# Optimization experiments

Measured on AMD Instinct MI355X. Metric: run time of the kernel, lower is better.

Reference implementation:

```python
import jax, jax.numpy as jnp
import numpy as np

S, B, C, H = 384, 2, 768, 12
CC = C // H

def setup_inputs() -> dict:
    key = jax.random.key(0)
    ks = jax.random.split(key, 8)
    x = jax.random.normal(ks[0], (S, B, C), dtype=jnp.float32)
    pe = jax.random.normal(ks[1], (S, S, B, C), dtype=jnp.float32)
    # causal mask: True where key index t > query index s (masked out)
    cm = (jnp.arange(S)[None, :] > jnp.arange(S)[:, None])[:, :, None]
    cm = jnp.broadcast_to(cm, (S, S, B))
    pm = jnp.zeros((S, S, B), dtype=bool)  # unused by the module's forward
    stdv = 1.0 / C ** 0.5
    qkv_w = jax.random.normal(ks[2], (3 * C, C), dtype=jnp.float32) * stdv
    qkv_b = jax.random.normal(ks[3], (3 * C,), dtype=jnp.float32) * stdv
    u = jax.random.uniform(ks[4], (C,), minval=-stdv, maxval=stdv, dtype=jnp.float32)
    w = jax.random.uniform(ks[5], (C,), minval=-stdv, maxval=stdv, dtype=jnp.float32)
    out_w = jax.random.normal(ks[6], (C, C), dtype=jnp.float32) * stdv
    out_b = jax.random.normal(ks[7], (C,), dtype=jnp.float32) * stdv
    return {"x": x, "pe": pe, "cm": cm, "pm": pm, "qkv_w": qkv_w,
            "qkv_b": qkv_b, "u": u, "w": w, "out_w": out_w, "out_b": out_b}

def reference(x, pe, cm, pm, qkv_w, qkv_b, u, w, out_w, out_b):
    s, b, c = x.shape
    qkv = x @ qkv_w.T + qkv_b                       # (s,b,3c)
    q, k, v = jnp.split(qkv, 3, axis=-1)
    q = q.reshape(s, b, H, CC)
    k = k.reshape(s, b, H, CC)
    v = v.reshape(s, b, H, CC)
    uh = u.reshape(1, 1, H, CC)
    wh = w.reshape(1, 1, H, CC)
    # content-content scores with global content bias u
    dd_ud = jnp.einsum('sbhc,tbhc->stbh', q + uh, k)
    # content-position scores against dense pairwise pe
    pe5 = pe.reshape(s, s, b, H, CC)
    dp_wp = jnp.einsum('sbhc,stbhc->stbh', q + wh, pe5)
    scale = 1.0 / CC ** 0.5
    a = (dd_ud + dp_wp) * scale
    a = jnp.where(cm[..., None], -jnp.inf, a)       # causal mask (intended)
    p = jax.nn.softmax(a, axis=1)                   # softmax over key axis t
    o = jnp.einsum('stbh,tbhc->sbhc', p, v).reshape(s, b, c)
    return o @ out_w.T + out_b
```

## Files before the change

kernel.cpp:

```cpp
#include <hip/hip_runtime.h>
#include <hip/hip_bf16.h>
#include <cstdint>

constexpr int kS  = 384;
constexpr int kB  = 2;
constexpr int kC  = 768;
constexpr int kH  = 12;
constexpr int kCC = 64;
constexpr int kHPB = 4;

typedef __attribute__((ext_vector_type(8))) short short8;
typedef __attribute__((ext_vector_type(4))) float f32x4;
typedef __attribute__((ext_vector_type(4))) unsigned short u16x4;
typedef const __attribute__((address_space(1))) unsigned int glb_u32_t;
typedef __attribute__((address_space(3))) unsigned int lds_u32_t;

static __device__ __forceinline__ ushort f2bf(float f) {
  __hip_bfloat16 h = __float2bfloat16(f);
  return *reinterpret_cast<ushort*>(&h);
}

__global__ __launch_bounds__(256) void convert_bf16(
    const float* __restrict__ x, const float* __restrict__ qw,
    const float* __restrict__ ow, ushort* __restrict__ xb,
    ushort* __restrict__ qwb, ushort* __restrict__ owb) {
  int idx = blockIdx.x * 256 + threadIdx.x;
  const float* src;
  ushort* dst;
  if (idx < 147456) {
    src = x; dst = xb;
  } else if (idx < 147456 + 442368) {
    idx -= 147456; src = qw; dst = qwb;
  } else {
    idx -= 589824; src = ow; dst = owb;
  }
  f32x4 v = *reinterpret_cast<const f32x4*>(src + (size_t)idx * 4);
  u16x4 o;
  o[0] = f2bf(v[0]); o[1] = f2bf(v[1]); o[2] = f2bf(v[2]); o[3] = f2bf(v[3]);
  *reinterpret_cast<u16x4*>(dst + (size_t)idx * 4) = o;
}

__global__ __launch_bounds__(256) void gemm_bf16_lds(
    const ushort* __restrict__ Abf, const ushort* __restrict__ Wbf,
    const float* __restrict__ bias, float* __restrict__ Cg,
    int M, int N, int K) {
  __shared__ ushort As[64 * 64];
  __shared__ ushort Ws[64 * 64];
  const int tid = threadIdx.x;
  const int m0 = blockIdx.y * 64, n0 = blockIdx.x * 64;
  const int wv = tid >> 6, l = tid & 63;
  const int wr = wv >> 1, wc = wv & 1;
  const int lr = l & 15, lk = l >> 4;

  f32x4 acc[2][2] = {{{0.f, 0.f, 0.f, 0.f}, {0.f, 0.f, 0.f, 0.f}},
                     {{0.f, 0.f, 0.f, 0.f}, {0.f, 0.f, 0.f, 0.f}}};

  for (int k0 = 0; k0 < K; k0 += 64) {
    __syncthreads();
#pragma unroll
    for (int j = 0; j < 2; ++j) {
      int cid = (j * 4 + wv) * 64 + l;
      int r = cid >> 3, c = cid & 7;
      int cs = c ^ (r & 7);
      const ushort* ga = Abf + (size_t)(m0 + r) * K + k0 + cs * 8;
      __builtin_amdgcn_global_load_lds((glb_u32_t*)ga,
                                       (lds_u32_t*)&As[(cid & ~63) * 8],
                                       16, 0, 0);
      const ushort* gw = Wbf + (size_t)(n0 + r) * K + k0 + cs * 8;
      __builtin_amdgcn_global_load_lds((glb_u32_t*)gw,
                                       (lds_u32_t*)&Ws[(cid & ~63) * 8],
                                       16, 0, 0);
    }
    __syncthreads();
#pragma unroll
    for (int ks = 0; ks < 2; ++ks) {
      short8 af[2], bw[2];
#pragma unroll
      for (int f = 0; f < 2; ++f) {
        int ra = wr * 32 + f * 16 + lr;
        int ca = (ks * 4 + lk) ^ (ra & 7);
        af[f] = *reinterpret_cast<const short8*>(&As[(ra * 8 + ca) * 8]);
        int rb = wc * 32 + f * 16 + lr;
        int cb = (ks * 4 + lk) ^ (rb & 7);
        bw[f] = *reinterpret_cast<const short8*>(&Ws[(rb * 8 + cb) * 8]);
      }
#pragma unroll
      for (int fr = 0; fr < 2; ++fr)
#pragma unroll
        for (int fc = 0; fc < 2; ++fc)
          acc[fr][fc] = __builtin_amdgcn_mfma_f32_16x16x32_bf16(
              af[fr], bw[fc], acc[fr][fc], 0, 0, 0);
    }
  }

#pragma unroll
  for (int fr = 0; fr < 2; ++fr)
#pragma unroll
    for (int fc = 0; fc < 2; ++fc)
#pragma unroll
      for (int j = 0; j < 4; ++j) {
        int m = m0 + wr * 32 + fr * 16 + lk * 4 + j;
        int n = n0 + wc * 32 + fc * 16 + lr;
        Cg[(size_t)m * N + n] = acc[fr][fc][j] + bias[n];
      }
}

__global__ __launch_bounds__(256, 6) void attn_kernel(
    const float* __restrict__ qkv, const float* __restrict__ pe,
    const float* __restrict__ u, const float* __restrict__ w,
    ushort* __restrict__ obf) {
  __shared__ float sc[kHPB][kS];

  const int bid = blockIdx.x;
  const int sb = bid / (kH / kHPB);
  const int hg = bid % (kH / kHPB);
  const int s = kS - 1 - (sb >> 1);
  const int b = sb & 1;
  const int wave = threadIdx.x >> 6;
  const int h = hg * kHPB + wave;
  const int lane = threadIdx.x & 63;
  const int tq = lane >> 4;
  const int cq = (lane & 15) * 4;
  const int ch = h * kCC + cq;
  const float scale = 0.125f;

  const int row = s * kB + b;
  const float4 q4 = *(const float4*)&qkv[(int64_t)row * 3 * kC + ch];
  const float4 u4 = *(const float4*)&u[ch];
  const float4 w4 = *(const float4*)&w[ch];
  float4 qu, qw;
  qu.x = q4.x + u4.x; qu.y = q4.y + u4.y; qu.z = q4.z + u4.z; qu.w = q4.w + u4.w;
  qw.x = q4.x + w4.x; qw.y = q4.y + w4.y; qw.z = q4.z + w4.z; qw.w = q4.w + w4.w;

  const float* kbase = qkv + (int64_t)b * 3 * kC + kC + ch;
  const float* vbase = qkv + (int64_t)b * 3 * kC + 2 * kC + ch;
  const float* pbase = pe + ((int64_t)s * kS * kB + b) * kC + ch;
  const int kstride = kB * 3 * kC;
  const int pstride = kB * kC;

  const int nfull = (s + 1) & ~15;

  int t0 = 0;
  for (; t0 < nfull; t0 += 16) {
    float4 k4[4];
    f32x4 p4[4];
#pragma unroll
    for (int i = 0; i < 4; ++i) {
      int t = t0 + i * 4 + tq;
      k4[i] = *(const float4*)&kbase[(int64_t)t * kstride];
      p4[i] = __builtin_nontemporal_load(
          (const f32x4*)&pbase[(int64_t)t * pstride]);
    }
#pragma unroll
    for (int i = 0; i < 4; ++i) {
      float r = qu.x * k4[i].x + qu.y * k4[i].y + qu.z * k4[i].z +
                qu.w * k4[i].w + qw.x * p4[i][0] + qw.y * p4[i][1] +
                qw.z * p4[i][2] + qw.w * p4[i][3];
      r += __shfl_xor(r, 1);
      r += __shfl_xor(r, 2);
      r += __shfl_xor(r, 4);
      r += __shfl_xor(r, 8);
      if ((lane & 15) == 0) sc[wave][t0 + i * 4 + tq] = r * scale;
    }
  }
  for (; t0 <= s; t0 += 4) {
    int t = t0 + tq;
    int tc = (t <= s) ? t : s;
    float4 k4 = *(const float4*)&kbase[(int64_t)tc * kstride];
    float4 p4 = *(const float4*)&pbase[(int64_t)tc * pstride];
    float r = qu.x * k4.x + qu.y * k4.y + qu.z * k4.z + qu.w * k4.w +
              qw.x * p4.x + qw.y * p4.y + qw.z * p4.z + qw.w * p4.w;
    r += __shfl_xor(r, 1);
    r += __shfl_xor(r, 2);
    r += __shfl_xor(r, 4);
    r += __shfl_xor(r, 8);
    if ((lane & 15) == 0 && t <= s) sc[wave][t] = r * scale;
  }
  __syncthreads();

  float mx = -1e30f;
  for (int t = lane; t <= s; t += 64) mx = fmaxf(mx, sc[wave][t]);
#pragma unroll
  for (int off = 32; off; off >>= 1) mx = fmaxf(mx, __shfl_xor(mx, off, 64));
  float sum = 0.f;
  for (int t = lane; t <= s; t += 64) {
    float e = __expf(sc[wave][t] - mx);
    sc[wave][t] = e;
    sum += e;
  }
#pragma unroll
  for (int off = 32; off; off >>= 1) sum += __shfl_xor(sum, off, 64);
  const float rden = 1.0f / sum;

  float4 oa = {0.f, 0.f, 0.f, 0.f};
  t0 = 0;
  for (; t0 < nfull; t0 += 16) {
    float4 v4[4];
    float p[4];
#pragma unroll
    for (int i = 0; i < 4; ++i) {
      int t = t0 + i * 4 + tq;
      v4[i] = *(const float4*)&vbase[(int64_t)t * kstride];
      p[i] = sc[wave][t];
    }
#pragma unroll
    for (int i = 0; i < 4; ++i) {
      oa.x += p[i] * v4[i].x; oa.y += p[i] * v4[i].y;
      oa.z += p[i] * v4[i].z; oa.w += p[i] * v4[i].w;
    }
  }
  for (; t0 <= s; t0 += 4) {
    int t = t0 + tq;
    if (t <= s) {
      float p = sc[wave][t];
      float4 v4 = *(const float4*)&vbase[(int64_t)t * kstride];
      oa.x += p * v4.x; oa.y += p * v4.y; oa.z += p * v4.z; oa.w += p * v4.w;
    }
  }
#pragma unroll
  for (int off = 16; off <= 32; off <<= 1) {
    oa.x += __shfl_xor(oa.x, off);
    oa.y += __shfl_xor(oa.y, off);
    oa.z += __shfl_xor(oa.z, off);
    oa.w += __shfl_xor(oa.w, off);
  }
  if (lane < 16) {
    u16x4 res;
    res[0] = f2bf(oa.x * rden); res[1] = f2bf(oa.y * rden);
    res[2] = f2bf(oa.z * rden); res[3] = f2bf(oa.w * rden);
    *reinterpret_cast<u16x4*>(&obf[(int64_t)row * kC + ch]) = res;
  }
}

extern "C" void kernel_launch(void* const* d_in, const int* in_sizes, int n_in,
                              void* d_out, int out_size, void* d_ws,
                              size_t ws_size, hipStream_t stream) {
  const float* x     = (const float*)d_in[0];
  const float* pe    = (const float*)d_in[1];
  const float* qkv_w = (const float*)d_in[4];
  const float* qkv_b = (const float*)d_in[5];
  const float* u     = (const float*)d_in[6];
  const float* w     = (const float*)d_in[7];
  const float* out_w = (const float*)d_in[8];
  const float* out_b = (const float*)d_in[9];
  float* out = (float*)d_out;

  char* wsb = (char*)d_ws;
  float*  qkv  = (float*)wsb;
  ushort* xb   = (ushort*)(wsb + 7077888);
  ushort* qwb  = (ushort*)(wsb + 8257536);
  ushort* owb  = (ushort*)(wsb + 11796480);
  ushort* obf  = (ushort*)(wsb + 12976128);

  convert_bf16<<<2880, 256, 0, stream>>>(x, qkv_w, out_w, xb, qwb, owb);

  gemm_bf16_lds<<<dim3(3 * kC / 64, kS * kB / 64), 256, 0, stream>>>(
      xb, qwb, qkv_b, qkv, kS * kB, 3 * kC, kC);

  attn_kernel<<<kS * kB * (kH / kHPB), kHPB * 64, 0, stream>>>(
      qkv, pe, u, w, obf);

  gemm_bf16_lds<<<dim3(kC / 64, kS * kB / 64), 256, 0, stream>>>(
      obf, owb, out_b, out, kS * kB, kC, kC);
}
```

Before: 137.2 us.

## Fuse attention into single-pass online softmax with DPP row reductions

Replaces the three-pass attention (scores into LDS, softmax, then PV) with a single streaming loop. The loop reads K, PE and V together and keeps an online softmax per lane group, with a lazy rescale threshold. The 16-lane score reductions move from __shfl_xor to DPP row operations, and the LDS buffer and block barrier are removed. In exchange, the loop is unrolled 2 instead of 4 per iteration, which means fewer loads in flight. Each step also pays for more exp calls and branches.

```diff
diff --git a/kernel.cpp b/kernel.cpp
--- a/kernel.cpp
+++ b/kernel.cpp
@@ -18,6 +18,20 @@
 static __device__ __forceinline__ ushort f2bf(float f) {
   __hip_bfloat16 h = __float2bfloat16(f);
   return *reinterpret_cast<ushort*>(&h);
+}
+
+template <int CTRL>
+static __device__ __forceinline__ float dpp_add(float x) {
+  int xi = __builtin_bit_cast(int, x);
+  int yi = __builtin_amdgcn_update_dpp(0, xi, CTRL, 0xF, 0xF, true);
+  return x + __builtin_bit_cast(float, yi);
+}
+static __device__ __forceinline__ float row16_sum(float x) {
+  x = dpp_add<0xB1>(x);
+  x = dpp_add<0x4E>(x);
+  x = dpp_add<0x124>(x);
+  x = dpp_add<0x128>(x);
+  return x;
 }
 
 __global__ __launch_bounds__(256) void convert_bf16(
@@ -109,8 +123,6 @@
     const float* __restrict__ qkv, const float* __restrict__ pe,
     const float* __restrict__ u, const float* __restrict__ w,
     ushort* __restrict__ obf) {
-  __shared__ float sc[kHPB][kS];
-
   const int bid = blockIdx.x;
   const int sb = bid / (kH / kHPB);
   const int hg = bid % (kH / kHPB);
@@ -125,12 +137,11 @@
   const float scale = 0.125f;
 
   const int row = s * kB + b;
-  const float4 q4 = *(const float4*)&qkv[(int64_t)row * 3 * kC + ch];
-  const float4 u4 = *(const float4*)&u[ch];
-  const float4 w4 = *(const float4*)&w[ch];
-  float4 qu, qw;
-  qu.x = q4.x + u4.x; qu.y = q4.y + u4.y; qu.z = q4.z + u4.z; qu.w = q4.w + u4.w;
-  qw.x = q4.x + w4.x; qw.y = q4.y + w4.y; qw.z = q4.z + w4.z; qw.w = q4.w + w4.w;
+  const f32x4 q4 = *(const f32x4*)&qkv[(int64_t)row * 3 * kC + ch];
+  const f32x4 u4 = *(const f32x4*)&u[ch];
+  const f32x4 w4 = *(const f32x4*)&w[ch];
+  const f32x4 qu = q4 + u4;
+  const f32x4 qw = q4 + w4;
 
   const float* kbase = qkv + (int64_t)b * 3 * kC + kC + ch;
   const float* vbase = qkv + (int64_t)b * 3 * kC + 2 * kC + ch;
@@ -138,96 +149,61 @@
   const int kstride = kB * 3 * kC;
   const int pstride = kB * kC;
 
-  const int nfull = (s + 1) & ~15;
-
-  int t0 = 0;
-  for (; t0 < nfull; t0 += 16) {
-    float4 k4[4];
-    f32x4 p4[4];
-#pragma unroll
-    for (int i = 0; i < 4; ++i) {
+  float m = -1e30f, l = 0.f;
+  f32x4 oa = {0.f, 0.f, 0.f, 0.f};
+
+  for (int t0 = 0; t0 <= s; t0 += 8) {
+    f32x4 k4[2], p4[2], v4[2];
+    int tt[2];
+#pragma unroll
+    for (int i = 0; i < 2; ++i) {
       int t = t0 + i * 4 + tq;
-      k4[i] = *(const float4*)&kbase[(int64_t)t * kstride];
+      tt[i] = t;
+      int tc = (t <= s) ? t : s;
+      k4[i] = *(const f32x4*)&kbase[(int64_t)tc * kstride];
       p4[i] = __builtin_nontemporal_load(
-          (const f32x4*)&pbase[(int64_t)t * pstride]);
-    }
-#pragma unroll
-    for (int i = 0; i < 4; ++i) {
-      float r = qu.x * k4[i].x + qu.y * k4[i].y + qu.z * k4[i].z +
-                qu.w * k4[i].w + qw.x * p4[i][0] + qw.y * p4[i][1] +
-                qw.z * p4[i][2] + qw.w * p4[i][3];
-      r += __shfl_xor(r, 1);
-      r += __shfl_xor(r, 2);
-      r += __shfl_xor(r, 4);
-      r += __shfl_xor(r, 8);
-      if ((lane & 15) == 0) sc[wave][t0 + i * 4 + tq] = r * scale;
-    }
-  }
-  for (; t0 <= s; t0 += 4) {
-    int t = t0 + tq;
-    int tc = (t <= s) ? t : s;
-    float4 k4 = *(const float4*)&kbase[(int64_t)tc * kstride];
-    float4 p4 = *(const float4*)&pbase[(int64_t)tc * pstride];
-    float r = qu.x * k4.x + qu.y * k4.y + qu.z * k4.z + qu.w * k4.w +
-              qw.x * p4.x + qw.y * p4.y + qw.z * p4.z + qw.w * p4.w;
-    r += __shfl_xor(r, 1);
-    r += __shfl_xor(r, 2);
-    r += __shfl_xor(r, 4);
-    r += __shfl_xor(r, 8);
-    if ((lane & 15) == 0 && t <= s) sc[wave][t] = r * scale;
-  }
-  __syncthreads();
-
-  float mx = -1e30f;
-  for (int t = lane; t <= s; t += 64) mx = fmaxf(mx, sc[wave][t]);
-#pragma unroll
-  for (int off = 32; off; off >>= 1) mx = fmaxf(mx, __shfl_xor(mx, off, 64));
-  float sum = 0.f;
-  for (int t = lane; t <= s; t += 64) {
-    float e = __expf(sc[wave][t] - mx);
-    sc[wave][t] = e;
-    sum += e;
-  }
-#pragma unroll
-  for (int off = 32; off; off >>= 1) sum += __shfl_xor(sum, off, 64);
-  const float rden = 1.0f / sum;
-
-  float4 oa = {0.f, 0.f, 0.f, 0.f};
-  t0 = 0;
-  for (; t0 < nfull; t0 += 16) {
-    float4 v4[4];
-    float p[4];
-#pragma unroll
-    for (int i = 0; i < 4; ++i) {
-      int t = t0 + i * 4 + tq;
-      v4[i] = *(const float4*)&vbase[(int64_t)t * kstride];
-      p[i] = sc[wave][t];
-    }
-#pragma unroll
-    for (int i = 0; i < 4; ++i) {
-      oa.x += p[i] * v4[i].x; oa.y += p[i] * v4[i].y;
-      oa.z += p[i] * v4[i].z; oa.w += p[i] * v4[i].w;
-    }
-  }
-  for (; t0 <= s; t0 += 4) {
-    int t = t0 + tq;
-    if (t <= s) {
-      float p = sc[wave][t];
-      float4 v4 = *(const float4*)&vbase[(int64_t)t * kstride];
-      oa.x += p * v4.x; oa.y += p * v4.y; oa.z += p * v4.z; oa.w += p * v4.w;
-    }
-  }
+          (const f32x4*)&pbase[(int64_t)tc * pstride]);
+      v4[i] = *(const f32x4*)&vbase[(int64_t)tc * kstride];
+    }
+#pragma unroll
+    for (int i = 0; i < 2; ++i) {
+      float r = qu[0] * k4[i][0] + qu[1] * k4[i][1] + qu[2] * k4[i][2] +
+                qu[3] * k4[i][3] + qw[0] * p4[i][0] + qw[1] * p4[i][1] +
+                qw[2] * p4[i][2] + qw[3] * p4[i][3];
+      r = row16_sum(r);
+      float y = (tt[i] <= s) ? r * scale : -1e30f;
+      if (y > m + 8.0f) {
+        float f = __expf(m - y);
+        l *= f;
+        oa[0] *= f; oa[1] *= f; oa[2] *= f; oa[3] *= f;
+        m = y;
+      }
+      float p = __expf(y - m);
+      l += p;
+      oa[0] += p * v4[i][0]; oa[1] += p * v4[i][1];
+      oa[2] += p * v4[i][2]; oa[3] += p * v4[i][3];
+    }
+  }
+
+  float mt = fmaxf(m, __shfl_xor(m, 16));
+  mt = fmaxf(mt, __shfl_xor(mt, 32));
+  const float f = __expf(m - mt);
+  float ls = l * f;
+  ls += __shfl_xor(ls, 16);
+  ls += __shfl_xor(ls, 32);
+  oa[0] *= f; oa[1] *= f; oa[2] *= f; oa[3] *= f;
 #pragma unroll
   for (int off = 16; off <= 32; off <<= 1) {
-    oa.x += __shfl_xor(oa.x, off);
-    oa.y += __shfl_xor(oa.y, off);
-    oa.z += __shfl_xor(oa.z, off);
-    oa.w += __shfl_xor(oa.w, off);
-  }
+    oa[0] += __shfl_xor(oa[0], off);
+    oa[1] += __shfl_xor(oa[1], off);
+    oa[2] += __shfl_xor(oa[2], off);
+    oa[3] += __shfl_xor(oa[3], off);
+  }
+  const float rden = 1.0f / ls;
   if (lane < 16) {
     u16x4 res;
-    res[0] = f2bf(oa.x * rden); res[1] = f2bf(oa.y * rden);
-    res[2] = f2bf(oa.z * rden); res[3] = f2bf(oa.w * rden);
+    res[0] = f2bf(oa[0] * rden); res[1] = f2bf(oa[1] * rden);
+    res[2] = f2bf(oa[2] * rden); res[3] = f2bf(oa[3] * rden);
     *reinterpret_cast<u16x4*>(&obf[(int64_t)row * kC + ch]) = res;
   }
 }
```

After: 146.2 us. +6.6%, slower.
